# Performance work log

Hardware: AMD Instinct MI355X
Metric: run time of the kernel (lower is better)

Reference implementation:

```python
import jax, jax.numpy as jnp
import numpy as np

SCALE = 64.0  # opt.train.scale
NUM_CLASSES = 10000

def setup_inputs() -> dict:
    key = jax.random.key(0)
    k1, k2 = jax.random.split(key)
    feature = jax.random.normal(k1, (8192, NUM_CLASSES), dtype=jnp.float32)
    label = jax.random.randint(k2, (8192,), 0, NUM_CLASSES, dtype=jnp.int64)
    return {"feature": feature, "label": label}

def reference(feature, label):
    # Original: one_hot scatter + elementwise multiply + global sum.
    # Mathematically: sum_i feature[i, label[i]] / scale, expressed as a gather.
    n = label.shape[0]
    picked = jnp.take_along_axis(feature, label[:, None].astype(jnp.int32), axis=1)  # [N,1]
    loss_center = 2.0 - 2.0 * (jnp.sum(picked) / SCALE) / n
    return loss_center
```

## Files before the change

### kernel.cpp

```cpp
#include <hip/hip_runtime.h>

#define N_ROWS 8192
#define N_COLS 10000
#define SCALE  64.0f
#define NBLK   128

__global__ __launch_bounds__(64) void center_partial(
    const float* __restrict__ feature,
    const int*   __restrict__ label,
    float*       __restrict__ partial) {
    const int i = blockIdx.x * 64 + threadIdx.x;
    const int l = label[i];
    float v = feature[(size_t)i * N_COLS + (size_t)l];

    #pragma unroll
    for (int off = 32; off > 0; off >>= 1)
        v += __shfl_down(v, off, 64);

    if (threadIdx.x == 0) partial[blockIdx.x] = v;
}

__global__ __launch_bounds__(64) void center_final(
    const float* __restrict__ partial,
    float*       __restrict__ out) {
    const int tid = threadIdx.x;
    float v = partial[tid] + partial[tid + 64];

    #pragma unroll
    for (int off = 32; off > 0; off >>= 1)
        v += __shfl_down(v, off, 64);

    if (tid == 0)
        out[0] = 2.0f - 2.0f * (v / SCALE) / (float)N_ROWS;
}

extern "C" void kernel_launch(void* const* d_in, const int* in_sizes, int n_in,
                              void* d_out, int out_size, void* d_ws, size_t ws_size,
                              hipStream_t stream) {
    const float* feature = (const float*)d_in[0];
    const int*   label   = (const int*)d_in[1];
    float*       out     = (float*)d_out;
    float*       partial = (float*)d_ws;

    center_partial<<<NBLK, 64, 0, stream>>>(feature, label, partial);
    center_final<<<1, 64, 0, stream>>>(partial, out);
}
```

Baseline: 349.6 us.

## Fuse partial and final reductions into a single 1024-thread block kernel

Replaces the two-kernel scheme (128 blocks of 64 threads computing partial sums, then a single-block final kernel) with one kernel launched as a single 1024-thread block. Each thread loads 8 labels via int4 vector loads and gathers 8 scattered feature elements, then reduces through wave shuffles and shared memory. This removes a kernel launch and the partial-sum round trip through global memory, at the cost of running all 8192 random gathers on one CU with less memory-level parallelism across the device.

```diff
diff --git a/kernel.cpp b/kernel.cpp
--- a/kernel.cpp
+++ b/kernel.cpp
@@ -3,35 +3,44 @@
 #define N_ROWS 8192
 #define N_COLS 10000
 #define SCALE  64.0f
-#define NBLK   128
 
-__global__ __launch_bounds__(64) void center_partial(
+__global__ __launch_bounds__(1024) void center_fused(
     const float* __restrict__ feature,
     const int*   __restrict__ label,
-    float*       __restrict__ partial) {
-    const int i = blockIdx.x * 64 + threadIdx.x;
-    const int l = label[i];
-    float v = feature[(size_t)i * N_COLS + (size_t)l];
+    float*       __restrict__ out) {
+    const int t = threadIdx.x;
+    const int base = t * 8;
+
+    const int4 l0 = ((const int4*)label)[2 * t];
+    const int4 l1 = ((const int4*)label)[2 * t + 1];
+
+    float v0 = feature[(size_t)(base + 0) * N_COLS + l0.x];
+    float v1 = feature[(size_t)(base + 1) * N_COLS + l0.y];
+    float v2 = feature[(size_t)(base + 2) * N_COLS + l0.z];
+    float v3 = feature[(size_t)(base + 3) * N_COLS + l0.w];
+    float v4 = feature[(size_t)(base + 4) * N_COLS + l1.x];
+    float v5 = feature[(size_t)(base + 5) * N_COLS + l1.y];
+    float v6 = feature[(size_t)(base + 6) * N_COLS + l1.z];
+    float v7 = feature[(size_t)(base + 7) * N_COLS + l1.w];
+
+    float s = ((v0 + v1) + (v2 + v3)) + ((v4 + v5) + (v6 + v7));
 
     #pragma unroll
     for (int off = 32; off > 0; off >>= 1)
-        v += __shfl_down(v, off, 64);
+        s += __shfl_down(s, off, 64);
 
-    if (threadIdx.x == 0) partial[blockIdx.x] = v;
-}
+    __shared__ float wsum[16];
+    if ((t & 63) == 0) wsum[t >> 6] = s;
+    __syncthreads();
 
-__global__ __launch_bounds__(64) void center_final(
-    const float* __restrict__ partial,
-    float*       __restrict__ out) {
-    const int tid = threadIdx.x;
-    float v = partial[tid] + partial[tid + 64];
-
-    #pragma unroll
-    for (int off = 32; off > 0; off >>= 1)
-        v += __shfl_down(v, off, 64);
-
-    if (tid == 0)
-        out[0] = 2.0f - 2.0f * (v / SCALE) / (float)N_ROWS;
+    if (t < 16) {
+        float x = wsum[t];
+        #pragma unroll
+        for (int off = 8; off > 0; off >>= 1)
+            x += __shfl_down(x, off, 16);
+        if (t == 0)
+            out[0] = 2.0f - 2.0f * (x / SCALE) / (float)N_ROWS;
+    }
 }
 
 extern "C" void kernel_launch(void* const* d_in, const int* in_sizes, int n_in,
@@ -40,8 +49,6 @@
     const float* feature = (const float*)d_in[0];
     const int*   label   = (const int*)d_in[1];
     float*       out     = (float*)d_out;
-    float*       partial = (float*)d_ws;
 
-    center_partial<<<NBLK, 64, 0, stream>>>(feature, label, partial);
-    center_final<<<1, 64, 0, stream>>>(partial, out);
+    center_fused<<<1, 1024, 0, stream>>>(feature, label, out);
 }
```

Result: slower. 367.4 us (+5.1%).
